# Optimization experiments

Measured on AMD Instinct MI355X. Metric: run time of the kernel, lower is better.

The kernel has to match this reference:

```python
import jax, jax.numpy as jnp
import numpy as np

N_NODES = 100000
N_REL = 3
HID = 256
LN_EPS = 1e-5
DENOM_EPS = 1e-8


def setup_inputs() -> dict:
    key = jax.random.key(0)
    ks = jax.random.split(key, 8)
    E = 300000
    return {
        "feat_text": jax.random.normal(ks[0], (N_NODES, 384), dtype=jnp.float32),
        "feat_image": jax.random.normal(ks[1], (N_NODES, 512), dtype=jnp.float32),
        "W_text": jax.random.normal(ks[2], (384, HID), dtype=jnp.float32) * 0.05,
        "W_image": jax.random.normal(ks[3], (512, HID), dtype=jnp.float32) * 0.05,
        "W_rel": jax.random.normal(ks[4], (N_REL, HID, HID), dtype=jnp.float32) * 0.05,
        "ln_gamma": jnp.ones((HID,), dtype=jnp.float32),
        "ln_beta": jnp.zeros((HID,), dtype=jnp.float32),
        "edge_weight": jax.random.uniform(ks[5], (E,), dtype=jnp.float32),
        "edge_index": jax.random.randint(ks[6], (2, E), 0, N_NODES),
        "edge_type": jax.random.randint(ks[7], (E,), 0, N_REL),
    }


def _layer_norm(x, gamma, beta):
    mu = jnp.mean(x, axis=-1, keepdims=True)
    var = jnp.mean(jnp.square(x - mu), axis=-1, keepdims=True)
    return (x - mu) * jax.lax.rsqrt(var + LN_EPS) * gamma + beta


def reference(feat_text, feat_image, W_text, W_image, W_rel, ln_gamma, ln_beta,
              edge_weight, edge_index, edge_type):
    # base embedding: mean of per-modality projections (fuse_mode='avg'), node 0 zeroed
    h0 = 0.5 * (feat_text @ W_text + feat_image @ W_image)  # [N, H]
    h0 = h0.at[0].set(0.0)

    src = edge_index[0]
    dst = edge_index[1]
    h_src = h0[src]  # [E, H] gather once, reused per relation

    aggregated = jnp.zeros_like(h0)
    for rel in range(N_REL):  # small fixed relation count
        w = jnp.where(edge_type == rel, edge_weight, 0.0)          # [E]
        msgs = (h_src @ W_rel[rel]) * w[:, None]                    # [E, H]
        agg_rel = jax.ops.segment_sum(msgs, dst, num_segments=N_NODES)   # [N, H]
        denom = jax.ops.segment_sum(w, dst, num_segments=N_NODES)        # [N]
        aggregated = aggregated + agg_rel / jnp.maximum(denom, DENOM_EPS)[:, None]

    # dropout=0.0 (identity)
    h1 = _layer_norm(h0 + aggregated, ln_gamma, ln_beta)
    h1 = h1.at[0].set(0.0)
    return h1
```

## Files before the change

### kernel.cpp

```cpp
#include <hip/hip_runtime.h>
#include <hip/hip_bf16.h>

#define HID 256
#define LN_EPS 1e-5f
#define DENOM_EPS 1e-8f

typedef __attribute__((ext_vector_type(8))) short short8;
typedef __attribute__((ext_vector_type(4))) float f32x4;

#define WP1_ELEMS (28 * 256 * 32)
#define WP2_ELEMS (24 * 256 * 32)

__device__ inline unsigned bfpk(float x, float y) {
    __hip_bfloat162 h = __float22bfloat162_rn(make_float2(x, y));
    return *reinterpret_cast<unsigned*>(&h);
}

__device__ inline void gld16(const void* g, void* l) {
    __builtin_amdgcn_global_load_lds(
        (const __attribute__((address_space(1))) void*)g,
        (__attribute__((address_space(3))) void*)l, 16, 0, 0);
}

__global__ __launch_bounds__(256) void kpack(
    const float* __restrict__ wt, const float* __restrict__ wi,
    const float* __restrict__ wrel,
    __hip_bfloat16* __restrict__ wp1, __hip_bfloat16* __restrict__ wp2)
{
    int idx = blockIdx.x * 256 + threadIdx.x;
    if (idx < WP1_ELEMS) {
        int kk = idx & 31, col = (idx >> 5) & 255, ks = idx >> 13;
        int k = ks * 32 + kk;
        float v = (k < 384) ? wt[k * 256 + col] : wi[(k - 384) * 256 + col];
        wp1[idx] = __float2bfloat16(v * 0.5f);
    } else {
        int j = idx - WP1_ELEMS;
        if (j < WP2_ELEMS) {
            int kk = j & 31, col = (j >> 5) & 255, ks = j >> 13;
            int k = ks * 32 + kk;
            wp2[j] = __float2bfloat16(wrel[k * 256 + col]);
        }
    }
}

__global__ __launch_bounds__(256) void kchain(
    const int* __restrict__ edst, int* __restrict__ head, int* __restrict__ nxt, int E)
{
    int e = blockIdx.x * 256 + threadIdx.x;
    if (e < E) nxt[e] = atomicExch(&head[edst[e]], e);
}

__global__ __launch_bounds__(256) void k2_gather(
    const float* __restrict__ h0, const int* __restrict__ esrc,
    const int* __restrict__ etype, const float* __restrict__ ew,
    const int* __restrict__ head, const int* __restrict__ nxt,
    __hip_bfloat16* __restrict__ S, int N)
{
    int gid = blockIdx.x * 256 + threadIdx.x;
    int d = gid >> 6;
    int lane = gid & 63;
    if (d >= N) return;

    f32x4 a0 = {0.f, 0.f, 0.f, 0.f}, a1 = a0, a2 = a0;
    float d0 = 0.f, d1 = 0.f, d2 = 0.f;

    int e = head[d];
    while (e >= 0) {
        int src = esrc[e];
        int ty = etype[e];
        float w = ew[e];
        const float4 h = *(const float4*)(h0 + (size_t)src * HID + lane * 4);
        f32x4 hw = {w * h.x, w * h.y, w * h.z, w * h.w};
        if (ty == 0)      { a0 += hw; d0 += w; }
        else if (ty == 1) { a1 += hw; d1 += w; }
        else              { a2 += hw; d2 += w; }
        e = nxt[e];
    }

    float i0 = 1.0f / fmaxf(d0, DENOM_EPS);
    float i1 = 1.0f / fmaxf(d1, DENOM_EPS);
    float i2 = 1.0f / fmaxf(d2, DENOM_EPS);
    __hip_bfloat16* row = S + (size_t)d * 768;
    uint2 p;
    p = make_uint2(bfpk(a0[0] * i0, a0[1] * i0), bfpk(a0[2] * i0, a0[3] * i0));
    *(uint2*)(row + 0   + lane * 4) = p;
    p = make_uint2(bfpk(a1[0] * i1, a1[1] * i1), bfpk(a1[2] * i1, a1[3] * i1));
    *(uint2*)(row + 256 + lane * 4) = p;
    p = make_uint2(bfpk(a2[0] * i2, a2[1] * i2), bfpk(a2[2] * i2, a2[3] * i2));
    *(uint2*)(row + 512 + lane * 4) = p;
}

template<int MODE>
__global__ __launch_bounds__(512) void kgemm(
    const float* __restrict__ a0, const float* __restrict__ a1,
    const __hip_bfloat16* __restrict__ Sb,
    const __hip_bfloat16* __restrict__ wp,
    const float* h0in, const float* __restrict__ gamma,
    const float* __restrict__ beta, float* out, int N)
{
    constexpr int NSTEPS = MODE ? 24 : 28;
    constexpr int TB = MODE ? 8192 : 16384;
    __shared__ __align__(16) unsigned char As[2][TB];
    __shared__ float redS[128][4];
    __shared__ float redQ[128][4];

    const int t = threadIdx.x;
    const int lane = t & 63;
    const int w = t >> 6;
    const int wr = w >> 2, wc = w & 3;
    const int m0 = blockIdx.x * 128;

    auto stageA = [&](int ks, int buf) {
        if constexpr (MODE == 0) {
#pragma unroll
            for (int j = 0; j < 2; ++j) {
                int r = 8 * (2 * w + j) + (lane >> 3);
                int grow = m0 + r; if (grow >= N) grow = m0;
                int q = (lane & 7) ^ (lane >> 3);
                const float* src = (ks < 12)
                    ? (a0 + (size_t)grow * 384 + ks * 32 + q * 4)
                    : (a1 + (size_t)grow * 512 + (ks - 12) * 32 + q * 4);
                gld16(src, As[buf] + (2 * w + j) * 1024);
            }
        } else {
            int r = 16 * w + (lane >> 2);
            int grow = m0 + r; if (grow >= N) grow = m0;
            int q = (lane & 3) ^ ((lane >> 3) & 3);
            const __hip_bfloat16* src = Sb + (size_t)grow * 768 + ks * 32 + q * 8;
            gld16(src, As[buf] + w * 1024);
        }
    };
    auto loadB = [&](short8* bf, int ks) {
#pragma unroll
        for (int fc = 0; fc < 4; ++fc)
            bf[fc] = *(const short8*)((const short*)wp +
                      (size_t)(ks * 256 + wc * 64 + fc * 16 + (lane & 15)) * 32 + (lane >> 4) * 8);
    };

    f32x4 acc[4][4];
#pragma unroll
    for (int i = 0; i < 4; ++i)
#pragma unroll
        for (int j = 0; j < 4; ++j) acc[i][j] = (f32x4){0.f, 0.f, 0.f, 0.f};

    short8 bfc[4], bfn[4];

    stageA(0, 0);
    loadB(bfc, 0);
    __syncthreads();

    const int g = lane >> 4;
    for (int ks = 0; ks < NSTEPS; ++ks) {
        const int cur = ks & 1;
        if (ks + 1 < NSTEPS) {
            stageA(ks + 1, cur ^ 1);
            loadB(bfn, ks + 1);
        }
        short8 af[4];
#pragma unroll
        for (int fr = 0; fr < 4; ++fr) {
            int r = wr * 64 + fr * 16 + (lane & 15);
            if constexpr (MODE == 0) {
                const unsigned char* base = As[cur] + r * 128;
                f32x4 lo = *(const f32x4*)(base + ((2 * g) ^ (r & 7)) * 16);
                f32x4 hi = *(const f32x4*)(base + ((2 * g + 1) ^ (r & 7)) * 16);
                union { short8 s; unsigned u[4]; } cv;
                cv.u[0] = bfpk(lo[0], lo[1]);
                cv.u[1] = bfpk(lo[2], lo[3]);
                cv.u[2] = bfpk(hi[0], hi[1]);
                cv.u[3] = bfpk(hi[2], hi[3]);
                af[fr] = cv.s;
            } else {
                af[fr] = *(const short8*)(As[cur] + r * 64 + ((g ^ ((r >> 1) & 3))) * 16);
            }
        }
#pragma unroll
        for (int fr = 0; fr < 4; ++fr)
#pragma unroll
            for (int fc = 0; fc < 4; ++fc)
                acc[fr][fc] = __builtin_amdgcn_mfma_f32_16x16x32_bf16(af[fr], bfc[fc], acc[fr][fc], 0, 0, 0);

        __syncthreads();
#pragma unroll
        for (int fc = 0; fc < 4; ++fc) bfc[fc] = bfn[fc];
    }

    const int rbase = m0 + wr * 64;
    const int cbase = wc * 64;

    if constexpr (MODE == 0) {
#pragma unroll
        for (int fr = 0; fr < 4; ++fr)
#pragma unroll
            for (int reg = 0; reg < 4; ++reg) {
                int grow = rbase + fr * 16 + (lane >> 4) * 4 + reg;
                if (grow >= N) continue;
#pragma unroll
                for (int fc = 0; fc < 4; ++fc) {
                    float vv = acc[fr][fc][reg];
                    if (grow == 0) vv = 0.f;
                    out[(size_t)grow * 256 + cbase + fc * 16 + (lane & 15)] = vv;
                }
            }
    } else {
#pragma unroll
        for (int fr = 0; fr < 4; ++fr)
#pragma unroll
            for (int reg = 0; reg < 4; ++reg) {
                int grow = rbase + fr * 16 + (lane >> 4) * 4 + reg;
                if (grow < N) {
#pragma unroll
                    for (int fc = 0; fc < 4; ++fc)
                        acc[fr][fc][reg] += h0in[(size_t)grow * 256 + cbase + fc * 16 + (lane & 15)];
                }
            }
#pragma unroll
        for (int fr = 0; fr < 4; ++fr)
#pragma unroll
            for (int reg = 0; reg < 4; ++reg) {
                float s = 0.f, q = 0.f;
#pragma unroll
                for (int fc = 0; fc < 4; ++fc) {
                    float vv = acc[fr][fc][reg];
                    s += vv; q += vv * vv;
                }
#pragma unroll
                for (int off = 1; off < 16; off <<= 1) {
                    s += __shfl_xor(s, off, 64);
                    q += __shfl_xor(q, off, 64);
                }
                if ((lane & 15) == 0) {
                    int rl = wr * 64 + fr * 16 + (lane >> 4) * 4 + reg;
                    redS[rl][wc] = s;
                    redQ[rl][wc] = q;
                }
            }
        __syncthreads();
        float g4[4], b4[4];
#pragma unroll
        for (int fc = 0; fc < 4; ++fc) {
            g4[fc] = gamma[cbase + fc * 16 + (lane & 15)];
            b4[fc] = beta[cbase + fc * 16 + (lane & 15)];
        }
#pragma unroll
        for (int fr = 0; fr < 4; ++fr)
#pragma unroll
            for (int reg = 0; reg < 4; ++reg) {
                int rl = wr * 64 + fr * 16 + (lane >> 4) * 4 + reg;
                int grow = m0 + rl;
                if (grow >= N) continue;
                float s = redS[rl][0] + redS[rl][1] + redS[rl][2] + redS[rl][3];
                float q = redQ[rl][0] + redQ[rl][1] + redQ[rl][2] + redQ[rl][3];
                float mu  = s * (1.f / 256.f);
                float var = q * (1.f / 256.f) - mu * mu;
                float rstd = rsqrtf(var + LN_EPS);
#pragma unroll
                for (int fc = 0; fc < 4; ++fc) {
                    float vv = (acc[fr][fc][reg] - mu) * rstd * g4[fc] + b4[fc];
                    if (grow == 0) vv = 0.f;
                    out[(size_t)grow * 256 + cbase + fc * 16 + (lane & 15)] = vv;
                }
            }
    }
}

extern "C" void kernel_launch(void* const* d_in, const int* in_sizes, int n_in,
                              void* d_out, int out_size, void* d_ws, size_t ws_size,
                              hipStream_t stream) {
    const int N = in_sizes[0] / 384;
    const int E = in_sizes[7];
    const float* ft    = (const float*)d_in[0];
    const float* fi    = (const float*)d_in[1];
    const float* wt    = (const float*)d_in[2];
    const float* wi    = (const float*)d_in[3];
    const float* wrel  = (const float*)d_in[4];
    const float* gamma = (const float*)d_in[5];
    const float* beta  = (const float*)d_in[6];
    const float* ew    = (const float*)d_in[7];
    const int*   eidx  = (const int*)d_in[8];
    const int*   etype = (const int*)d_in[9];
    float* out = (float*)d_out;

    __hip_bfloat16* S = (__hip_bfloat16*)d_ws;
    int* head = (int*)((char*)d_ws + (size_t)N * 768 * 2);
    int* nxt  = head + N;
    __hip_bfloat16* wp1 = (__hip_bfloat16*)(nxt + E);
    __hip_bfloat16* wp2 = wp1 + WP1_ELEMS;

    hipMemsetAsync(head, 0xFF, (size_t)N * sizeof(int), stream);

    kpack<<<(WP1_ELEMS + WP2_ELEMS + 255) / 256, 256, 0, stream>>>(wt, wi, wrel, wp1, wp2);

    kchain<<<(E + 255) / 256, 256, 0, stream>>>(eidx + E, head, nxt, E);

    const int gblocks = (N + 127) / 128;
    kgemm<0><<<gblocks, 512, 0, stream>>>(ft, fi, nullptr, wp1, nullptr, nullptr, nullptr, out, N);

    const int wblocks = (N + 3) / 4;
    k2_gather<<<wblocks, 256, 0, stream>>>(out, eidx, etype, ew, head, nxt, S, N);

    kgemm<1><<<gblocks, 512, 0, stream>>>(nullptr, nullptr, S, wp2, out, gamma, beta, out, N);
}
```

Measured before the change: 355.0 us.

## Shrink GEMM tiles to 64 rows with 4 waves and triple-buffered LDS

The fused projection and relation GEMM kernels move from 128-row tiles with 8 waves to 64-row tiles with 4 waves, each wave covering 64 output columns. A-tile staging becomes a 3-deep LDS ring with a single barrier per k-step, and B fragments are loaded in-step instead of prefetched into registers. The aim is lower LDS and register use per block, so more blocks fit per CU for occupancy and latency hiding. In exchange each block has less reuse of B across rows, so there is more global or cache traffic for weights, and the synchronisation pattern depends on the 3-buffer ring being correct.

```diff
diff --git a/kernel.cpp b/kernel.cpp
--- a/kernel.cpp
+++ b/kernel.cpp
@@ -91,7 +91,7 @@
 }
 
 template<int MODE>
-__global__ __launch_bounds__(512) void kgemm(
+__global__ __launch_bounds__(256, 4) void kgemm(
     const float* __restrict__ a0, const float* __restrict__ a1,
     const __hip_bfloat16* __restrict__ Sb,
     const __hip_bfloat16* __restrict__ wp,
@@ -99,69 +99,64 @@
     const float* __restrict__ beta, float* out, int N)
 {
     constexpr int NSTEPS = MODE ? 24 : 28;
-    constexpr int TB = MODE ? 8192 : 16384;
-    __shared__ __align__(16) unsigned char As[2][TB];
-    __shared__ float redS[128][4];
-    __shared__ float redQ[128][4];
+    constexpr int TB = MODE ? 4096 : 8192;
+    __shared__ __align__(16) unsigned char As[3][TB];
+    __shared__ float redS[MODE ? 64 : 1][4];
+    __shared__ float redQ[MODE ? 64 : 1][4];
 
     const int t = threadIdx.x;
     const int lane = t & 63;
     const int w = t >> 6;
-    const int wr = w >> 2, wc = w & 3;
-    const int m0 = blockIdx.x * 128;
+    const int m0 = blockIdx.x * 64;
+    const int g = lane >> 4;
 
     auto stageA = [&](int ks, int buf) {
         if constexpr (MODE == 0) {
 #pragma unroll
             for (int j = 0; j < 2; ++j) {
-                int r = 8 * (2 * w + j) + (lane >> 3);
+                int slot = j * 4 + w;
+                int r = slot * 8 + (lane >> 3);
                 int grow = m0 + r; if (grow >= N) grow = m0;
                 int q = (lane & 7) ^ (lane >> 3);
                 const float* src = (ks < 12)
                     ? (a0 + (size_t)grow * 384 + ks * 32 + q * 4)
                     : (a1 + (size_t)grow * 512 + (ks - 12) * 32 + q * 4);
-                gld16(src, As[buf] + (2 * w + j) * 1024);
+                gld16(src, As[buf] + slot * 1024);
             }
         } else {
-            int r = 16 * w + (lane >> 2);
+            int r = w * 16 + (lane >> 2);
             int grow = m0 + r; if (grow >= N) grow = m0;
             int q = (lane & 3) ^ ((lane >> 3) & 3);
             const __hip_bfloat16* src = Sb + (size_t)grow * 768 + ks * 32 + q * 8;
             gld16(src, As[buf] + w * 1024);
         }
     };
-    auto loadB = [&](short8* bf, int ks) {
+
+    f32x4 acc[4][4];
+#pragma unroll
+    for (int i = 0; i < 4; ++i)
+#pragma unroll
+        for (int j = 0; j < 4; ++j) acc[i][j] = (f32x4){0.f, 0.f, 0.f, 0.f};
+
+    stageA(0, 0);
+
+    for (int ks = 0; ks < NSTEPS; ++ks) {
+        if (ks + 1 < NSTEPS) stageA(ks + 1, (ks + 1) % 3);
+        short8 bf[4];
 #pragma unroll
         for (int fc = 0; fc < 4; ++fc)
             bf[fc] = *(const short8*)((const short*)wp +
-                      (size_t)(ks * 256 + wc * 64 + fc * 16 + (lane & 15)) * 32 + (lane >> 4) * 8);
-    };
-
-    f32x4 acc[4][4];
-#pragma unroll
-    for (int i = 0; i < 4; ++i)
-#pragma unroll
-        for (int j = 0; j < 4; ++j) acc[i][j] = (f32x4){0.f, 0.f, 0.f, 0.f};
-
-    short8 bfc[4], bfn[4];
-
-    stageA(0, 0);
-    loadB(bfc, 0);
-    __syncthreads();
-
-    const int g = lane >> 4;
-    for (int ks = 0; ks < NSTEPS; ++ks) {
-        const int cur = ks & 1;
-        if (ks + 1 < NSTEPS) {
-            stageA(ks + 1, cur ^ 1);
-            loadB(bfn, ks + 1);
-        }
+                      (size_t)(ks * 256 + w * 64 + fc * 16 + (lane & 15)) * 32 + g * 8);
+
+        __syncthreads();
+
+        const unsigned char* Ab = As[ks % 3];
         short8 af[4];
 #pragma unroll
         for (int fr = 0; fr < 4; ++fr) {
-            int r = wr * 64 + fr * 16 + (lane & 15);
+            int r = fr * 16 + (lane & 15);
             if constexpr (MODE == 0) {
-                const unsigned char* base = As[cur] + r * 128;
+                const unsigned char* base = Ab + r * 128;
                 f32x4 lo = *(const f32x4*)(base + ((2 * g) ^ (r & 7)) * 16);
                 f32x4 hi = *(const f32x4*)(base + ((2 * g + 1) ^ (r & 7)) * 16);
                 union { short8 s; unsigned u[4]; } cv;
@@ -171,29 +166,24 @@
                 cv.u[3] = bfpk(hi[2], hi[3]);
                 af[fr] = cv.s;
             } else {
-                af[fr] = *(const short8*)(As[cur] + r * 64 + ((g ^ ((r >> 1) & 3))) * 16);
+                af[fr] = *(const short8*)(Ab + r * 64 + (g ^ ((r >> 1) & 3)) * 16);
             }
         }
 #pragma unroll
         for (int fr = 0; fr < 4; ++fr)
 #pragma unroll
             for (int fc = 0; fc < 4; ++fc)
-                acc[fr][fc] = __builtin_amdgcn_mfma_f32_16x16x32_bf16(af[fr], bfc[fc], acc[fr][fc], 0, 0, 0);
-
-        __syncthreads();
-#pragma unroll
-        for (int fc = 0; fc < 4; ++fc) bfc[fc] = bfn[fc];
-    }
-
-    const int rbase = m0 + wr * 64;
-    const int cbase = wc * 64;
+                acc[fr][fc] = __builtin_amdgcn_mfma_f32_16x16x32_bf16(af[fr], bf[fc], acc[fr][fc], 0, 0, 0);
+    }
+
+    const int cbase = w * 64;
 
     if constexpr (MODE == 0) {
 #pragma unroll
         for (int fr = 0; fr < 4; ++fr)
 #pragma unroll
             for (int reg = 0; reg < 4; ++reg) {
-                int grow = rbase + fr * 16 + (lane >> 4) * 4 + reg;
+                int grow = m0 + fr * 16 + g * 4 + reg;
                 if (grow >= N) continue;
 #pragma unroll
                 for (int fc = 0; fc < 4; ++fc) {
@@ -207,7 +197,7 @@
         for (int fr = 0; fr < 4; ++fr)
 #pragma unroll
             for (int reg = 0; reg < 4; ++reg) {
-                int grow = rbase + fr * 16 + (lane >> 4) * 4 + reg;
+                int grow = m0 + fr * 16 + g * 4 + reg;
                 if (grow < N) {
 #pragma unroll
                     for (int fc = 0; fc < 4; ++fc)
@@ -230,9 +220,9 @@
                     q += __shfl_xor(q, off, 64);
                 }
                 if ((lane & 15) == 0) {
-                    int rl = wr * 64 + fr * 16 + (lane >> 4) * 4 + reg;
-                    redS[rl][wc] = s;
-                    redQ[rl][wc] = q;
+                    int rl = fr * 16 + g * 4 + reg;
+                    redS[rl][w] = s;
+                    redQ[rl][w] = q;
                 }
             }
         __syncthreads();
@@ -246,7 +236,7 @@
         for (int fr = 0; fr < 4; ++fr)
 #pragma unroll
             for (int reg = 0; reg < 4; ++reg) {
-                int rl = wr * 64 + fr * 16 + (lane >> 4) * 4 + reg;
+                int rl = fr * 16 + g * 4 + reg;
                 int grow = m0 + rl;
                 if (grow >= N) continue;
                 float s = redS[rl][0] + redS[rl][1] + redS[rl][2] + redS[rl][3];
@@ -293,11 +283,11 @@
 
     kchain<<<(E + 255) / 256, 256, 0, stream>>>(eidx + E, head, nxt, E);
 
-    const int gblocks = (N + 127) / 128;
-    kgemm<0><<<gblocks, 512, 0, stream>>>(ft, fi, nullptr, wp1, nullptr, nullptr, nullptr, out, N);
+    const int gblocks = (N + 63) / 64;
+    kgemm<0><<<gblocks, 256, 0, stream>>>(ft, fi, nullptr, wp1, nullptr, nullptr, nullptr, out, N);
 
     const int wblocks = (N + 3) / 4;
     k2_gather<<<wblocks, 256, 0, stream>>>(out, eidx, etype, ew, head, nxt, S, N);
 
-    kgemm<1><<<gblocks, 512, 0, stream>>>(nullptr, nullptr, S, wp2, out, gamma, beta, out, N);
-}
+    kgemm<1><<<gblocks, 256, 0, stream>>>(nullptr, nullptr, S, wp2, out, gamma, beta, out, N);
+}
```

After: 337.7 us. -4.9%, faster.
